# Optimization experiments

Hardware: AMD Instinct MI355X
Metric: run time of the kernel (lower is better)

Reference implementation:

```python
import jax, jax.numpy as jnp
import numpy as np

N_EMBD = 1024
N_HEAD = 16
HEAD_DIM = N_EMBD // N_HEAD
EPS = 1e-5


def setup_inputs() -> dict:
    key = jax.random.key(0)
    ks = jax.random.split(key, 6)
    B, S, D = 2, 2048, N_EMBD
    s = 0.02
    return {
        "x": jax.random.normal(ks[0], (B, S, D), jnp.float32),
        "ln1_g": jnp.ones((D,), jnp.float32),
        "ln1_b": jnp.zeros((D,), jnp.float32),
        "w_attn": jax.random.normal(ks[1], (D, 3 * D), jnp.float32) * s,
        "b_attn": jnp.zeros((3 * D,), jnp.float32),
        "w_attn_proj": jax.random.normal(ks[2], (D, D), jnp.float32) * s,
        "b_attn_proj": jnp.zeros((D,), jnp.float32),
        "ln2_g": jnp.ones((D,), jnp.float32),
        "ln2_b": jnp.zeros((D,), jnp.float32),
        "w_fc": jax.random.normal(ks[3], (D, 4 * D), jnp.float32) * s,
        "b_fc": jnp.zeros((4 * D,), jnp.float32),
        "w_fc_proj": jax.random.normal(ks[4], (4 * D, D), jnp.float32) * s,
        "b_fc_proj": jnp.zeros((D,), jnp.float32),
    }


def _layernorm(x, g, b):
    mu = jnp.mean(x, axis=-1, keepdims=True)
    var = jnp.mean(jnp.square(x - mu), axis=-1, keepdims=True)
    return (x - mu) * jax.lax.rsqrt(var + EPS) * g + b


def _block(x, ln1_g, ln1_b, w_attn, b_attn, w_attn_proj, b_attn_proj,
           ln2_g, ln2_b, w_fc, b_fc, w_fc_proj, b_fc_proj):
    B, S, D = x.shape
    h = _layernorm(x, ln1_g, ln1_b)
    qkv = h @ w_attn + b_attn                       # [B,S,3D]
    q, k, v = jnp.split(qkv, 3, axis=-1)
    # [B,H,S,hd]
    q = q.reshape(B, S, N_HEAD, HEAD_DIM).transpose(0, 2, 1, 3)
    k = k.reshape(B, S, N_HEAD, HEAD_DIM).transpose(0, 2, 1, 3)
    v = v.reshape(B, S, N_HEAD, HEAD_DIM).transpose(0, 2, 1, 3)
    scores = jnp.einsum("bhqd,bhkd->bhqk", q, k) / jnp.sqrt(
        jnp.asarray(HEAD_DIM, x.dtype))
    causal = jnp.tril(jnp.ones((S, S), bool))
    scores = jnp.where(causal, scores, -jnp.inf)
    attn = jax.nn.softmax(scores, axis=-1)
    out = jnp.einsum("bhqk,bhkd->bhqd", attn, v)    # [B,H,S,hd]
    out = out.transpose(0, 2, 1, 3).reshape(B, S, D)
    x = x + (out @ w_attn_proj + b_attn_proj)
    h2 = _layernorm(x, ln2_g, ln2_b)
    m = jax.nn.gelu(h2 @ w_fc + b_fc, approximate=False)
    x = x + (m @ w_fc_proj + b_fc_proj)
    return x


def reference(x, ln1_g, ln1_b, w_attn, b_attn, w_attn_proj, b_attn_proj,
              ln2_g, ln2_b, w_fc, b_fc, w_fc_proj, b_fc_proj):
    return _block(x, ln1_g, ln1_b, w_attn, b_attn, w_attn_proj, b_attn_proj,
                  ln2_g, ln2_b, w_fc, b_fc, w_fc_proj, b_fc_proj)
```

## Files before the change

kernel.cpp:

```cpp
#include <hip/hip_runtime.h>
#include <hip/hip_bf16.h>
#include <math.h>

typedef __bf16 bf16_t;
typedef bf16_t bf16x8 __attribute__((ext_vector_type(8)));
typedef float f32x4 __attribute__((ext_vector_type(4)));
typedef float f32x16 __attribute__((ext_vector_type(16)));
typedef unsigned short u16;
typedef u16 ushort8 __attribute__((ext_vector_type(8)));

static __device__ __forceinline__ u16 f2bf(float f) {
    unsigned u = __builtin_bit_cast(unsigned, f);
    u += 0x7FFFu + ((u >> 16) & 1u);
    return (u16)(u >> 16);
}
static __device__ __forceinline__ float bf2f(u16 v) {
    unsigned u = (unsigned)v << 16;
    return __builtin_bit_cast(float, u);
}

static __device__ __forceinline__ int swz_row(int s, int lane) {
    const int t = (lane & 7) ^ ((lane >> 3) & 7);
    return s * 16 + ((lane >> 3) << 1) + (t >> 2);
}
static __device__ __forceinline__ int swz_kk(int lane) {
    const int t = (lane & 7) ^ ((lane >> 3) & 7);
    return (t & 3) << 3;
}
static __device__ __forceinline__ int swz_rd(int R, int c) {
    return (R >> 1) * 64 + (((((R & 1) << 2) + c) ^ ((R >> 1) & 7)) << 3);
}

static __device__ __forceinline__ int aidx32(int R, int s, int lane) {
    return R * 64 + (((((s << 1) | (lane >> 5))) ^ (R & 7)) << 3);
}

__global__ __launch_bounds__(256) void ln_kernel(
    const float* __restrict__ x, const float* __restrict__ g,
    const float* __restrict__ be, u16* __restrict__ out)
{
    const int row = blockIdx.x;
    const int tid = threadIdx.x;
    const float4 v = ((const float4*)(x + (long)row * 1024))[tid];
    float s = v.x + v.y + v.z + v.w;
#pragma unroll
    for (int d = 32; d >= 1; d >>= 1) s += __shfl_xor(s, d);
    __shared__ float r1[4], r2[4];
    if ((tid & 63) == 0) r1[tid >> 6] = s;
    __syncthreads();
    const float mean = (r1[0] + r1[1] + r1[2] + r1[3]) * (1.0f / 1024.0f);
    const float dx = v.x - mean, dy = v.y - mean, dz = v.z - mean, dw = v.w - mean;
    float sq = dx * dx + dy * dy + dz * dz + dw * dw;
#pragma unroll
    for (int d = 32; d >= 1; d >>= 1) sq += __shfl_xor(sq, d);
    if ((tid & 63) == 0) r2[tid >> 6] = sq;
    __syncthreads();
    const float var = (r2[0] + r2[1] + r2[2] + r2[3]) * (1.0f / 1024.0f);
    const float rstd = rsqrtf(var + 1e-5f);
    const float4 gg = ((const float4*)g)[tid];
    const float4 bb = ((const float4*)be)[tid];
    ushort4 o;
    o.x = f2bf(dx * rstd * gg.x + bb.x);
    o.y = f2bf(dy * rstd * gg.y + bb.y);
    o.z = f2bf(dz * rstd * gg.z + bb.z);
    o.w = f2bf(dw * rstd * gg.w + bb.w);
    *(ushort4*)&out[(long)row * 1024 + tid * 4] = o;
}

__global__ __launch_bounds__(256) void tcvt_kernel(
    const float* __restrict__ in, u16* __restrict__ outT, int R, int C)
{
    __shared__ float tile[32][33];
    const int tx = threadIdx.x, ty = threadIdx.y;
    const int c0 = blockIdx.x * 32, r0 = blockIdx.y * 32;
#pragma unroll
    for (int i = 0; i < 4; ++i)
        tile[ty + i * 8][tx] = in[(long)(r0 + ty + i * 8) * C + c0 + tx];
    __syncthreads();
#pragma unroll
    for (int i = 0; i < 4; ++i)
        outT[(long)(c0 + ty + i * 8) * R + r0 + tx] = f2bf(tile[tx][ty + i * 8]);
}

template <int EPI, int DP>
static __device__ __forceinline__ void gemm128_body(
    const u16* __restrict__ A, const u16* __restrict__ Bt,
    const float* __restrict__ bias, const float* __restrict__ resid,
    void* __restrict__ C, int M, int N, int Kloop, int ldA)
{
    constexpr int MR = 4, NR = 4;
    constexpr int LPW = 4;
    __shared__ __align__(16) u16 As[DP][128 * 32];
    __shared__ __align__(16) u16 Bs[DP][128 * 32];
    const int tid = threadIdx.x;
    const int lane = tid & 63;
    const int w = tid >> 6;
    const int wm = w >> 1, wn = w & 1;
    const int bm = blockIdx.x, bn = blockIdx.y;
    f32x4 acc[MR][NR] = {};

    const u16* Ablk = A + (long)bm * 128 * ldA;
    const u16* Bblk = Bt + (long)bn * 128 * ldA;
    const int nt = Kloop >> 5;

    long soff[2];
#pragma unroll
    for (int i = 0; i < 2; ++i)
        soff[i] = (long)swz_row(w * 2 + i, lane) * ldA + swz_kk(lane);

    auto stage = [&](int buf, int kb) {
#pragma unroll
        for (int i = 0; i < 2; ++i) {
            __builtin_amdgcn_global_load_lds(
                (const __attribute__((address_space(1))) void*)(Ablk + soff[i] + kb),
                (__attribute__((address_space(3))) void*)(&As[buf][(w * 2 + i) * 512]),
                16, 0, 0);
            __builtin_amdgcn_global_load_lds(
                (const __attribute__((address_space(1))) void*)(Bblk + soff[i] + kb),
                (__attribute__((address_space(3))) void*)(&Bs[buf][(w * 2 + i) * 512]),
                16, 0, 0);
        }
    };

#pragma unroll
    for (int s = 0; s < DP - 1; ++s) stage(s, s << 5);

    for (int t = 0; t < nt; ++t) {
        const int cur = t % DP;
        if (t + DP - 2 < nt) {
            asm volatile("s_waitcnt vmcnt(%0)" :: "i"((DP - 2) * LPW) : "memory");
        } else if (t + 1 < nt) {
            asm volatile("s_waitcnt vmcnt(%0)" :: "i"(LPW) : "memory");
        } else {
            asm volatile("s_waitcnt vmcnt(0)" ::: "memory");
        }
        __builtin_amdgcn_s_barrier();
        asm volatile("" ::: "memory");

        if (t + DP - 1 < nt) stage((t + DP - 1) % DP, (t + DP - 1) << 5);

        bf16x8 af[MR], bfr[NR];
        const int c = lane >> 4;
#pragma unroll
        for (int m = 0; m < MR; ++m)
            af[m] = *(const bf16x8*)&As[cur][swz_rd(wm * 64 + m * 16 + (lane & 15), c)];
#pragma unroll
        for (int n = 0; n < NR; ++n)
            bfr[n] = *(const bf16x8*)&Bs[cur][swz_rd(wn * 64 + n * 16 + (lane & 15), c)];
#pragma unroll
        for (int m = 0; m < MR; ++m)
#pragma unroll
            for (int n = 0; n < NR; ++n)
                acc[m][n] = __builtin_amdgcn_mfma_f32_16x16x32_bf16(af[m], bfr[n], acc[m][n], 0, 0, 0);
        asm volatile("" ::: "memory");
    }

    const int rowBase = bm * 128 + wm * 64;
    const int colBase = bn * 128 + wn * 64;
#pragma unroll
    for (int n = 0; n < NR; ++n) {
        const int col = colBase + n * 16 + (lane & 15);
        const float bv = bias ? bias[col] : 0.0f;
#pragma unroll
        for (int m = 0; m < MR; ++m) {
#pragma unroll
            for (int r = 0; r < 4; ++r) {
                const int row = rowBase + m * 16 + (lane >> 4) * 4 + r;
                float v = acc[m][n][r] + bv;
                if constexpr (EPI == 1) {
                    const float u = v + 0.044715f * v * v * v;
                    v = v / (1.0f + __expf(-1.5957691216057308f * u));
                }
                if constexpr (EPI == 3) {
                    if (col < 1024) v *= 0.125f;
                }
                if constexpr (EPI == 2) {
                    ((float*)C)[(long)row * N + col] = v + resid[(long)row * N + col];
                } else {
                    ((u16*)C)[(long)row * N + col] = f2bf(v);
                }
            }
        }
    }
}

template <int EPI>
static __device__ __forceinline__ void gemm64w32_body(
    const u16* __restrict__ A, const u16* __restrict__ Bt,
    const float* __restrict__ bias, const float* __restrict__ resid,
    void* __restrict__ C, int M, int N, int K)
{
    __shared__ __align__(16) u16 As[2][64 * 64];
    const int tid = threadIdx.x;
    const int lane = tid & 63;
    const int w = tid >> 6;
    const int bm = blockIdx.x, bn = blockIdx.y;
    f32x16 acc[2] = {};

    const u16* Ablk = A + (long)bm * 64 * K;
    const u16* Bblk = Bt + (long)bn * 128 * K;
    const int nt = K >> 6;

    const u16* bpB = Bblk + (long)(w * 32 + (lane & 31)) * K + ((lane >> 5) << 3);

    long soffA[2];
#pragma unroll
    for (int i = 0; i < 2; ++i)
        soffA[i] = (long)((w * 2 + i) * 8 + (lane >> 3)) * K
                 + (((lane & 7) ^ (lane >> 3)) << 3);

    auto stageA = [&](int buf, int kb) {
#pragma unroll
        for (int i = 0; i < 2; ++i)
            __builtin_amdgcn_global_load_lds(
                (const __attribute__((address_space(1))) void*)(Ablk + soffA[i] + kb),
                (__attribute__((address_space(3))) void*)(&As[buf][(w * 2 + i) * 512]),
                16, 0, 0);
    };

    ushort8 Ba[4], Bb[4];
    stageA(0, 0);
    __builtin_amdgcn_sched_barrier(0);
    asm volatile("global_load_dwordx4 %0, %1, off" : "=v"(Ba[0]) : "v"(bpB));
    asm volatile("global_load_dwordx4 %0, %1, off" : "=v"(Ba[1]) : "v"(bpB + 16));
    asm volatile("global_load_dwordx4 %0, %1, off" : "=v"(Ba[2]) : "v"(bpB + 32));
    asm volatile("global_load_dwordx4 %0, %1, off" : "=v"(Ba[3]) : "v"(bpB + 48));

    auto iter = [&](int t, ushort8 (&cur)[4], ushort8 (&pf)[4]) {
        asm volatile("s_waitcnt vmcnt(4)" ::: "memory");
        __builtin_amdgcn_s_barrier();
        asm volatile("" ::: "memory");
        const bool more = (t + 1 < nt);
        if (more) {
            stageA((t + 1) & 1, (t + 1) << 6);
            __builtin_amdgcn_sched_barrier(0);
            const u16* p = bpB + ((long)(t + 1) << 6);
            asm volatile("global_load_dwordx4 %0, %1, off" : "=v"(pf[0]) : "v"(p));
            asm volatile("global_load_dwordx4 %0, %1, off" : "=v"(pf[1]) : "v"(p + 16));
            asm volatile("global_load_dwordx4 %0, %1, off" : "=v"(pf[2]) : "v"(p + 32));
            asm volatile("global_load_dwordx4 %0, %1, off" : "=v"(pf[3]) : "v"(p + 48));
        }
        bf16x8 af[2][4];
#pragma unroll
        for (int m = 0; m < 2; ++m)
#pragma unroll
            for (int s = 0; s < 4; ++s)
                af[m][s] = *(const bf16x8*)&As[t & 1][aidx32(m * 32 + (lane & 31), s, lane)];
        if (more) asm volatile("s_waitcnt vmcnt(6)" ::: "memory");
        else      asm volatile("s_waitcnt vmcnt(0)" ::: "memory");
        __builtin_amdgcn_sched_barrier(0);
        bf16x8 b[4];
#pragma unroll
        for (int i = 0; i < 4; ++i) b[i] = __builtin_bit_cast(bf16x8, cur[i]);
#pragma unroll
        for (int s = 0; s < 4; ++s)
#pragma unroll
            for (int m = 0; m < 2; ++m)
                acc[m] = __builtin_amdgcn_mfma_f32_32x32x16_bf16(af[m][s], b[s], acc[m], 0, 0, 0);
        asm volatile("" ::: "memory");
    };

    for (int t = 0; t < nt; t += 2) {
        iter(t, Ba, Bb);
        iter(t + 1, Bb, Ba);
    }

    const int rowBase = bm * 64;
    const int col = bn * 128 + w * 32 + (lane & 31);
    const float bv = bias[col];
#pragma unroll
    for (int m = 0; m < 2; ++m) {
#pragma unroll
        for (int reg = 0; reg < 16; ++reg) {
            const int row = rowBase + m * 32 + (reg & 3) + 8 * (reg >> 2) + 4 * (lane >> 5);
            float v = acc[m][reg] + bv;
            if constexpr (EPI == 2) {
                ((float*)C)[(long)row * N + col] = v + resid[(long)row * N + col];
            } else {
                ((u16*)C)[(long)row * N + col] = f2bf(v);
            }
        }
    }
}

__global__ __launch_bounds__(256) void gemm_qkv(
    const u16* A, const u16* Bt, const float* bias, const float* resid,
    void* C, int M, int N, int K) { gemm128_body<3, 3>(A, Bt, bias, resid, C, M, N, K, K); }
__global__ __launch_bounds__(256) void gemm_fc(
    const u16* A, const u16* Bt, const float* bias, const float* resid,
    void* C, int M, int N, int K) { gemm128_body<1, 3>(A, Bt, bias, resid, C, M, N, K, K); }
__global__ __launch_bounds__(256) void gemm_ap(
    const u16* A, const u16* Bt, const float* bias, const float* resid,
    void* C, int M, int N, int K) { gemm64w32_body<2>(A, Bt, bias, resid, C, M, N, K); }

__global__ __launch_bounds__(256) void gemm_fp_part(
    const u16* A, const u16* Bt, u16* P, int M, int N, int Kfull)
{
    const int kh = blockIdx.z;
    gemm128_body<0, 3>(A + kh * 2048, Bt + kh * 2048, nullptr, nullptr,
                       P + (size_t)kh * 4096 * 1024, M, N, 2048, Kfull);
}

__global__ __launch_bounds__(256) void reduce_fp(
    const u16* __restrict__ p0, const u16* __restrict__ p1,
    const float* __restrict__ bias, float* __restrict__ out)
{
    const long e = ((long)blockIdx.x * 256 + threadIdx.x) * 8;
    const int col = (int)(e & 1023);
    const ushort8 a = *(const ushort8*)&p0[e];
    const ushort8 b = *(const ushort8*)&p1[e];
    const float4 bi0 = *(const float4*)&bias[col];
    const float4 bi1 = *(const float4*)&bias[col + 4];
    float4 r0 = *(const float4*)&out[e];
    float4 r1 = *(const float4*)&out[e + 4];
    r0.x += bf2f(a[0]) + bf2f(b[0]) + bi0.x;
    r0.y += bf2f(a[1]) + bf2f(b[1]) + bi0.y;
    r0.z += bf2f(a[2]) + bf2f(b[2]) + bi0.z;
    r0.w += bf2f(a[3]) + bf2f(b[3]) + bi0.w;
    r1.x += bf2f(a[4]) + bf2f(b[4]) + bi1.x;
    r1.y += bf2f(a[5]) + bf2f(b[5]) + bi1.y;
    r1.z += bf2f(a[6]) + bf2f(b[6]) + bi1.z;
    r1.w += bf2f(a[7]) + bf2f(b[7]) + bi1.w;
    *(float4*)&out[e] = r0;
    *(float4*)&out[e + 4] = r1;
}

__global__ __launch_bounds__(256) void attn_kernel(
    const u16* __restrict__ qkv, u16* __restrict__ outb)
{
    const int S = 2048;
    const int flat = blockIdx.x + 16 * blockIdx.y;
    const int work = (flat & 7) * 64 + (flat >> 3);
    const int ipair = work & 15;
    const int bh = work >> 4;
    const int b = bh >> 4, h = bh & 15;
    const int tid = threadIdx.x, lane = tid & 63, w = tid >> 6;
    __shared__ __align__(16) u16 Ks[2][64 * 72];
    __shared__ __align__(16) u16 Vs[2][64 * 72];
    __shared__ __align__(16) u16 Ps[4][16 * 72];

    const long base = (long)b * S * 3072;
    const int rstage = tid >> 3;
    const int cg = (tid & 7) * 8;
    const int sw = cg;
    const u16* kbase = qkv + base + 1024 + h * 64 + cg;
    const u16* vbase = qkv + base + 2048 + h * 64 + cg;

    for (int half = 0; half < 2; ++half) {
        const int qt = half ? 31 - ipair : ipair;
        const int q0 = qt * 64;

        bf16x8 qf[2];
        {
            const int qrow = q0 + w * 16 + (lane & 15);
#pragma unroll
            for (int c = 0; c < 2; ++c)
                qf[c] = *(const bf16x8*)&qkv[base + (long)qrow * 3072 + h * 64 + c * 32 + (lane >> 4) * 8];
        }

        f32x4 Of[4] = {};
        float m = -1e30f, l = 0.0f;

        ushort8 kr[2], vr[2];
#pragma unroll
        for (int it = 0; it < 2; ++it) {
            const long ro = (long)(it * 32 + rstage) * 3072;
            kr[it] = *(const ushort8*)&kbase[ro];
            vr[it] = *(const ushort8*)&vbase[ro];
        }
        __syncthreads();
#pragma unroll
        for (int it = 0; it < 2; ++it) {
            const int r = it * 32 + rstage;
            *(ushort8*)&Ks[0][r * 72 + cg] = kr[it];
#pragma unroll
            for (int j = 0; j < 8; ++j)
                Vs[0][(cg + j) * 72 + (r ^ sw)] = vr[it][j];
        }

        for (int kt = 0; kt <= qt; ++kt) {
            const int cur = kt & 1;
            if (kt < qt) {
#pragma unroll
                for (int it = 0; it < 2; ++it) {
                    const long ro = (long)((kt + 1) * 64 + it * 32 + rstage) * 3072;
                    kr[it] = *(const ushort8*)&kbase[ro];
                    vr[it] = *(const ushort8*)&vbase[ro];
                }
            }
            __syncthreads();

            f32x4 Sf[4] = {};
            __builtin_amdgcn_s_setprio(1);
#pragma unroll
            for (int f = 0; f < 4; ++f) {
#pragma unroll
                for (int c = 0; c < 2; ++c) {
                    const bf16x8 kf = *(const bf16x8*)&Ks[cur][(f * 16 + (lane & 15)) * 72 + c * 32 + (lane >> 4) * 8];
                    Sf[f] = __builtin_amdgcn_mfma_f32_16x16x32_bf16(kf, qf[c], Sf[f], 0, 0, 0);
                }
            }
            __builtin_amdgcn_s_setprio(0);
            if (kt == qt) {
                const int ql = w * 16 + (lane & 15);
#pragma unroll
                for (int f = 0; f < 4; ++f) {
#pragma unroll
                    for (int r = 0; r < 4; ++r) {
                        const int kvl = f * 16 + ((lane >> 4) << 2) + r;
                        if (kvl > ql) Sf[f][r] = -1e30f;
                    }
                }
            }
            float pmax = Sf[0][0];
#pragma unroll
            for (int f = 0; f < 4; ++f)
#pragma unroll
                for (int r = 0; r < 4; ++r) pmax = fmaxf(pmax, Sf[f][r]);
            if (!__all(pmax <= m + 8.0f)) {
                float pm = pmax;
                pm = fmaxf(pm, __shfl_xor(pm, 16));
                pm = fmaxf(pm, __shfl_xor(pm, 32));
                const float mnew = fmaxf(m, pm);
                const float sc = __expf(m - mnew);
                m = mnew;
                l *= sc;
                float sco[4];
#pragma unroll
                for (int r = 0; r < 4; ++r)
                    sco[r] = __shfl(sc, ((lane >> 4) << 2) + r);
#pragma unroll
                for (int f = 0; f < 4; ++f)
#pragma unroll
                    for (int r = 0; r < 4; ++r) Of[f][r] *= sco[r];
            }
            float osum = 0.0f;
#pragma unroll
            for (int f = 0; f < 4; ++f)
#pragma unroll
                for (int r = 0; r < 4; ++r) {
                    const float e = __expf(Sf[f][r] - m);
                    Sf[f][r] = e;
                    osum += e;
                }
            l += osum;
#pragma unroll
            for (int f = 0; f < 4; ++f) {
                const unsigned lo = (unsigned)f2bf(Sf[f][0]) | ((unsigned)f2bf(Sf[f][1]) << 16);
                const unsigned hi = (unsigned)f2bf(Sf[f][2]) | ((unsigned)f2bf(Sf[f][3]) << 16);
                uint2 pk; pk.x = lo; pk.y = hi;
                *(uint2*)&Ps[w][(lane & 15) * 72 + f * 16 + ((lane >> 4) << 2)] = pk;
            }
            __builtin_amdgcn_s_setprio(1);
#pragma unroll
            for (int f = 0; f < 4; ++f) {
                const int hd = f * 16 + (lane & 15);
#pragma unroll
                for (int c = 0; c < 2; ++c) {
                    const int k0 = c * 32 + (lane >> 4) * 8;
                    const bf16x8 pa = *(const bf16x8*)&Ps[w][(lane & 15) * 72 + k0];
                    const bf16x8 vb = *(const bf16x8*)&Vs[cur][hd * 72 + (k0 ^ (hd & 56))];
                    Of[f] = __builtin_amdgcn_mfma_f32_16x16x32_bf16(pa, vb, Of[f], 0, 0, 0);
                }
            }
            __builtin_amdgcn_s_setprio(0);
            if (kt < qt) {
#pragma unroll
                for (int it = 0; it < 2; ++it) {
                    const int r = it * 32 + rstage;
                    *(ushort8*)&Ks[cur ^ 1][r * 72 + cg] = kr[it];
#pragma unroll
                    for (int j = 0; j < 8; ++j)
                        Vs[cur ^ 1][(cg + j) * 72 + (r ^ sw)] = vr[it][j];
                }
            }
        }

        float lt = l;
        lt += __shfl_xor(lt, 16);
        lt += __shfl_xor(lt, 32);
        const float linv = 1.0f / lt;
        float inv[4];
#pragma unroll
        for (int r = 0; r < 4; ++r)
            inv[r] = __shfl(linv, ((lane >> 4) << 2) + r);
#pragma unroll
        for (int f = 0; f < 4; ++f) {
            const int col = h * 64 + f * 16 + (lane & 15);
#pragma unroll
            for (int r = 0; r < 4; ++r) {
                const int qrow = q0 + w * 16 + (lane >> 4) * 4 + r;
                outb[((long)b * S + qrow) * 1024 + col] = f2bf(Of[f][r] * inv[r]);
            }
        }
    }
}

extern "C" void kernel_launch(void* const* d_in, const int* in_sizes, int n_in,
                              void* d_out, int out_size, void* d_ws, size_t ws_size,
                              hipStream_t stream) {
    const float* x      = (const float*)d_in[0];
    const float* ln1_g  = (const float*)d_in[1];
    const float* ln1_b  = (const float*)d_in[2];
    const float* w_attn = (const float*)d_in[3];
    const float* b_attn = (const float*)d_in[4];
    const float* w_ap   = (const float*)d_in[5];
    const float* b_ap   = (const float*)d_in[6];
    const float* ln2_g  = (const float*)d_in[7];
    const float* ln2_b  = (const float*)d_in[8];
    const float* w_fc   = (const float*)d_in[9];
    const float* b_fc   = (const float*)d_in[10];
    const float* w_fp   = (const float*)d_in[11];
    const float* b_fp   = (const float*)d_in[12];
    float* out = (float*)d_out;

    const int R = 4096;
    char* p = (char*)d_ws;
    u16*   wTa  = (u16*)(p);
    u16*   wTap = (u16*)(p + 6291456);
    u16*   wTfc = (u16*)(p + 8388608);
    u16*   wTfp = (u16*)(p + 16777216);
    u16*   hao  = (u16*)(p + 25165824);
    u16*   qkv  = (u16*)(p + 33554432);
    u16*   mb   = hao;
    u16*   h2   = wTa;
    u16*   fpp  = (u16*)(p);
    float* x1   = out;

    const dim3 tb(32, 8);
    tcvt_kernel<<<dim3(3072 / 32, 1024 / 32), tb, 0, stream>>>(w_attn, wTa, 1024, 3072);
    tcvt_kernel<<<dim3(1024 / 32, 1024 / 32), tb, 0, stream>>>(w_ap, wTap, 1024, 1024);
    tcvt_kernel<<<dim3(4096 / 32, 1024 / 32), tb, 0, stream>>>(w_fc, wTfc, 1024, 4096);
    tcvt_kernel<<<dim3(1024 / 32, 4096 / 32), tb, 0, stream>>>(w_fp, wTfp, 4096, 1024);

    ln_kernel<<<R, 256, 0, stream>>>(x, ln1_g, ln1_b, hao);
    gemm_qkv<<<dim3(32, 24), 256, 0, stream>>>(hao, wTa, b_attn, nullptr, qkv, R, 3072, 1024);
    attn_kernel<<<dim3(16, 32), 256, 0, stream>>>(qkv, hao);
    gemm_ap<<<dim3(64, 8), 256, 0, stream>>>(hao, wTap, b_ap, x, x1, R, 1024, 1024);
    ln_kernel<<<R, 256, 0, stream>>>(x1, ln2_g, ln2_b, h2);
    gemm_fc<<<dim3(32, 32), 256, 0, stream>>>(h2, wTfc, b_fc, nullptr, mb, R, 4096, 1024);
    gemm_fp_part<<<dim3(32, 8, 2), 256, 0, stream>>>(mb, wTfp, fpp, R, 1024, 4096);
    reduce_fp<<<2048, 256, 0, stream>>>(fpp, fpp + (size_t)4096 * 1024, b_fp, out);
}
```

Before: 260.5 us.

## Add 256x256-tile 8-wave GEMM with interleaved prefetch for QKV and FC

Adds a new GEMM body with 256x256 block tiles, 512 threads (8 waves) and a triple-buffered LDS pipeline. It issues global-to-LDS loads in four stages spread between MFMA groups, separated by barriers and s_setprio around the MFMAs. The goal is more operand reuse per LDS load and better overlap of memory with matrix math for the QKV and FC projections. The trade-off is much larger per-block LDS and register use, and far fewer blocks: 192 for QKV and 256 for FC, which may leave some CUs idle. The fused GELU and q-scale epilogues move out of the old 128-tile body into the new one.

```diff
diff --git a/kernel.cpp b/kernel.cpp
--- a/kernel.cpp
+++ b/kernel.cpp
@@ -82,6 +82,152 @@
         outT[(long)(c0 + ty + i * 8) * R + r0 + tx] = f2bf(tile[tx][ty + i * 8]);
 }
 
+template <int EPI>
+static __device__ __forceinline__ void gemm256_body(
+    const u16* __restrict__ A, const u16* __restrict__ Bt,
+    const float* __restrict__ bias, const float* __restrict__ resid,
+    void* __restrict__ C, int M, int N, int K)
+{
+    __shared__ __align__(16) u16 As[3][256 * 32];
+    __shared__ __align__(16) u16 Bs[3][256 * 32];
+    const int tid = threadIdx.x;
+    const int lane = tid & 63;
+    const int w = tid >> 6;
+    const int wm = w >> 2, wn = w & 3;
+    const int bm = blockIdx.x, bn = blockIdx.y;
+    f32x4 acc[8][4] = {};
+
+    const u16* Ablk = A + (long)bm * 256 * K;
+    const u16* Bblk = Bt + (long)bn * 256 * K;
+    const int NT = K >> 5;
+
+    long soff[2];
+#pragma unroll
+    for (int i = 0; i < 2; ++i)
+        soff[i] = (long)swz_row(w * 2 + i, lane) * K + swz_kk(lane);
+
+    auto stageA = [&](int buf, int kb, int i) {
+        __builtin_amdgcn_global_load_lds(
+            (const __attribute__((address_space(1))) void*)(Ablk + soff[i] + kb),
+            (__attribute__((address_space(3))) void*)(&As[buf][(w * 2 + i) * 512]),
+            16, 0, 0);
+    };
+    auto stageB = [&](int buf, int kb, int i) {
+        __builtin_amdgcn_global_load_lds(
+            (const __attribute__((address_space(1))) void*)(Bblk + soff[i] + kb),
+            (__attribute__((address_space(3))) void*)(&Bs[buf][(w * 2 + i) * 512]),
+            16, 0, 0);
+    };
+
+    stageA(0, 0, 0);  stageA(0, 0, 1);  stageB(0, 0, 0);  stageB(0, 0, 1);
+    stageA(1, 32, 0); stageA(1, 32, 1); stageB(1, 32, 0); stageB(1, 32, 1);
+
+    int buf = 0;
+    for (int t = 0; t < NT; ++t) {
+        int nbuf = buf + 2; if (nbuf >= 3) nbuf -= 3;
+        const int kb2 = (t + 2) << 5;
+        const bool pf = (t + 2) < NT;
+        const int c = lane >> 4;
+        bf16x8 af[8], bfr[4];
+
+        if (pf) stageA(nbuf, kb2, 0);
+        if (pf)               asm volatile("s_waitcnt vmcnt(5)" ::: "memory");
+        else if (t + 1 < NT)  asm volatile("s_waitcnt vmcnt(4)" ::: "memory");
+        else                  asm volatile("s_waitcnt vmcnt(0)" ::: "memory");
+        __builtin_amdgcn_s_barrier();
+        asm volatile("" ::: "memory");
+#pragma unroll
+        for (int f = 0; f < 4; ++f)
+            af[f] = *(const bf16x8*)&As[buf][swz_rd(wm * 128 + f * 16 + (lane & 15), c)];
+#pragma unroll
+        for (int n = 0; n < 2; ++n)
+            bfr[n] = *(const bf16x8*)&Bs[buf][swz_rd(wn * 64 + n * 16 + (lane & 15), c)];
+        __builtin_amdgcn_s_setprio(1);
+#pragma unroll
+        for (int f = 0; f < 4; ++f)
+#pragma unroll
+            for (int n = 0; n < 2; ++n)
+                acc[f][n] = __builtin_amdgcn_mfma_f32_16x16x32_bf16(af[f], bfr[n], acc[f][n], 0, 0, 0);
+        __builtin_amdgcn_s_setprio(0);
+        asm volatile("" ::: "memory");
+
+#pragma unroll
+        for (int n = 2; n < 4; ++n)
+            bfr[n] = *(const bf16x8*)&Bs[buf][swz_rd(wn * 64 + n * 16 + (lane & 15), c)];
+        if (pf) stageA(nbuf, kb2, 1);
+        __builtin_amdgcn_s_barrier();
+        asm volatile("" ::: "memory");
+        __builtin_amdgcn_s_setprio(1);
+#pragma unroll
+        for (int f = 0; f < 4; ++f)
+#pragma unroll
+            for (int n = 2; n < 4; ++n)
+                acc[f][n] = __builtin_amdgcn_mfma_f32_16x16x32_bf16(af[f], bfr[n], acc[f][n], 0, 0, 0);
+        __builtin_amdgcn_s_setprio(0);
+        asm volatile("" ::: "memory");
+
+#pragma unroll
+        for (int f = 4; f < 8; ++f)
+            af[f] = *(const bf16x8*)&As[buf][swz_rd(wm * 128 + f * 16 + (lane & 15), c)];
+        if (pf) stageB(nbuf, kb2, 0);
+        __builtin_amdgcn_s_barrier();
+        asm volatile("" ::: "memory");
+        __builtin_amdgcn_s_setprio(1);
+#pragma unroll
+        for (int f = 4; f < 8; ++f)
+#pragma unroll
+            for (int n = 0; n < 2; ++n)
+                acc[f][n] = __builtin_amdgcn_mfma_f32_16x16x32_bf16(af[f], bfr[n], acc[f][n], 0, 0, 0);
+        __builtin_amdgcn_s_setprio(0);
+        asm volatile("" ::: "memory");
+
+        if (pf) stageB(nbuf, kb2, 1);
+        __builtin_amdgcn_s_barrier();
+        asm volatile("" ::: "memory");
+        __builtin_amdgcn_s_setprio(1);
+#pragma unroll
+        for (int f = 4; f < 8; ++f)
+#pragma unroll
+            for (int n = 2; n < 4; ++n)
+                acc[f][n] = __builtin_amdgcn_mfma_f32_16x16x32_bf16(af[f], bfr[n], acc[f][n], 0, 0, 0);
+        __builtin_amdgcn_s_setprio(0);
+        asm volatile("" ::: "memory");
+
+        buf = (buf == 2) ? 0 : buf + 1;
+    }
+
+    const int rowBase = bm * 256 + wm * 128;
+    const int colBase = bn * 256 + wn * 64;
+#pragma unroll
+    for (int n = 0; n < 4; ++n) {
+        const int col = colBase + n * 16 + (lane & 15);
+        const float bv = bias[col];
+#pragma unroll
+        for (int m = 0; m < 8; ++m) {
+#pragma unroll
+            for (int r = 0; r < 4; ++r) {
+                const int row = rowBase + m * 16 + (lane >> 4) * 4 + r;
+                float v = acc[m][n][r] + bv;
+                if constexpr (EPI == 1) {
+                    const float u = v + 0.044715f * v * v * v;
+                    v = v / (1.0f + __expf(-1.5957691216057308f * u));
+                }
+                if constexpr (EPI == 3) {
+                    if (col < 1024) v *= 0.125f;
+                }
+                ((u16*)C)[(long)row * N + col] = f2bf(v);
+            }
+        }
+    }
+}
+
+__global__ __launch_bounds__(512, 2) void gemm_qkv(
+    const u16* A, const u16* Bt, const float* bias, const float* resid,
+    void* C, int M, int N, int K) { gemm256_body<3>(A, Bt, bias, resid, C, M, N, K); }
+__global__ __launch_bounds__(512, 2) void gemm_fc(
+    const u16* A, const u16* Bt, const float* bias, const float* resid,
+    void* C, int M, int N, int K) { gemm256_body<1>(A, Bt, bias, resid, C, M, N, K); }
+
 template <int EPI, int DP>
 static __device__ __forceinline__ void gemm128_body(
     const u16* __restrict__ A, const u16* __restrict__ Bt,
@@ -167,13 +313,6 @@
             for (int r = 0; r < 4; ++r) {
                 const int row = rowBase + m * 16 + (lane >> 4) * 4 + r;
                 float v = acc[m][n][r] + bv;
-                if constexpr (EPI == 1) {
-                    const float u = v + 0.044715f * v * v * v;
-                    v = v / (1.0f + __expf(-1.5957691216057308f * u));
-                }
-                if constexpr (EPI == 3) {
-                    if (col < 1024) v *= 0.125f;
-                }
                 if constexpr (EPI == 2) {
                     ((float*)C)[(long)row * N + col] = v + resid[(long)row * N + col];
                 } else {
@@ -283,12 +422,6 @@
     }
 }
 
-__global__ __launch_bounds__(256) void gemm_qkv(
-    const u16* A, const u16* Bt, const float* bias, const float* resid,
-    void* C, int M, int N, int K) { gemm128_body<3, 3>(A, Bt, bias, resid, C, M, N, K, K); }
-__global__ __launch_bounds__(256) void gemm_fc(
-    const u16* A, const u16* Bt, const float* bias, const float* resid,
-    void* C, int M, int N, int K) { gemm128_body<1, 3>(A, Bt, bias, resid, C, M, N, K, K); }
 __global__ __launch_bounds__(256) void gemm_ap(
     const u16* A, const u16* Bt, const float* bias, const float* resid,
     void* C, int M, int N, int K) { gemm64w32_body<2>(A, Bt, bias, resid, C, M, N, K); }
@@ -534,11 +667,11 @@
     tcvt_kernel<<<dim3(1024 / 32, 4096 / 32), tb, 0, stream>>>(w_fp, wTfp, 4096, 1024);
 
     ln_kernel<<<R, 256, 0, stream>>>(x, ln1_g, ln1_b, hao);
-    gemm_qkv<<<dim3(32, 24), 256, 0, stream>>>(hao, wTa, b_attn, nullptr, qkv, R, 3072, 1024);
+    gemm_qkv<<<dim3(16, 12), 512, 0, stream>>>(hao, wTa, b_attn, nullptr, qkv, R, 3072, 1024);
     attn_kernel<<<dim3(16, 32), 256, 0, stream>>>(qkv, hao);
     gemm_ap<<<dim3(64, 8), 256, 0, stream>>>(hao, wTap, b_ap, x, x1, R, 1024, 1024);
     ln_kernel<<<R, 256, 0, stream>>>(x1, ln2_g, ln2_b, h2);
-    gemm_fc<<<dim3(32, 32), 256, 0, stream>>>(h2, wTfc, b_fc, nullptr, mb, R, 4096, 1024);
+    gemm_fc<<<dim3(16, 16), 512, 0, stream>>>(h2, wTfc, b_fc, nullptr, mb, R, 4096, 1024);
     gemm_fp_part<<<dim3(32, 8, 2), 256, 0, stream>>>(mb, wTfp, fpp, R, 1024, 4096);
     reduce_fp<<<2048, 256, 0, stream>>>(fpp, fpp + (size_t)4096 * 1024, b_fp, out);
 }
```

After: 263.9 us. Within noise of the previous version (+1.3%).
